# Kernel tuning notes

Measured on AMD Instinct MI355X. Metric: run time of the kernel, lower is better.

## Reference

```python
import jax, jax.numpy as jnp
import numpy as np

DIM = 1024
NUM_HEADS = 16
HEAD_DIM = DIM // NUM_HEADS
SCALE = HEAD_DIM ** -0.5


def setup_inputs() -> dict:
    key = jax.random.key(0)
    ks = jax.random.split(key, 11)
    B, N, M = 8, 1024, 1024
    s = DIM ** -0.5  # init scale for weights
    return {
        "x": jax.random.normal(ks[0], (B, N, DIM), jnp.float32),
        "context": jax.random.normal(ks[1], (B, M, DIM), jnp.float32),
        "Wq": jax.random.normal(ks[2], (DIM, DIM), jnp.float32) * s,
        "bq": jax.random.normal(ks[3], (DIM,), jnp.float32) * 0.01,
        "Wk": jax.random.normal(ks[4], (DIM, DIM), jnp.float32) * s,
        "bk": jax.random.normal(ks[5], (DIM,), jnp.float32) * 0.01,
        "Wv": jax.random.normal(ks[6], (DIM, DIM), jnp.float32) * s,
        "bv": jax.random.normal(ks[7], (DIM,), jnp.float32) * 0.01,
        "Wo": jax.random.normal(ks[8], (DIM, DIM), jnp.float32) * s,
        "bo": jax.random.normal(ks[9], (DIM,), jnp.float32) * 0.01,
    }


def reference(x, context, Wq, bq, Wk, bk, Wv, bv, Wo, bo):
    B, N, _ = x.shape
    M = context.shape[1]
    # Linear projections (torch Linear: x @ W.T + b; here W stored as [in, out])
    q = x @ Wq + bq            # [B, N, DIM]
    k = context @ Wk + bk      # [B, M, DIM]
    v = context @ Wv + bv      # [B, M, DIM]
    # split heads: b n (h d) -> b h n d
    q = q.reshape(B, N, NUM_HEADS, HEAD_DIM).transpose(0, 2, 1, 3)
    k = k.reshape(B, M, NUM_HEADS, HEAD_DIM).transpose(0, 2, 1, 3)
    v = v.reshape(B, M, NUM_HEADS, HEAD_DIM).transpose(0, 2, 1, 3)
    dots = jnp.einsum('bhnd,bhmd->bhnm', q, k) * SCALE
    attn = jax.nn.softmax(dots, axis=-1)
    out = jnp.einsum('bhnm,bhmd->bhnd', attn, v)   # [B, H, N, d]
    out = out.transpose(0, 2, 1, 3).reshape(B, N, DIM)  # b h n d -> b n (h d)
    return out @ Wo + bo
```

## Files before the change

### kernel.cpp

```cpp
#include <hip/hip_runtime.h>

typedef unsigned short u16;
typedef __attribute__((ext_vector_type(8))) short bf16x8;
typedef __attribute__((ext_vector_type(4))) float f32x4;
typedef __attribute__((ext_vector_type(16))) float f32x16;
typedef __attribute__((ext_vector_type(4))) unsigned u32x4;

#define MFMA16 __builtin_amdgcn_mfma_f32_16x16x32_bf16
#define MFMA32 __builtin_amdgcn_mfma_f32_32x32x16_bf16

__device__ __forceinline__ u16 f2b(float f) {
  unsigned u = __builtin_bit_cast(unsigned, f);
  u = (u + 0x7fffu + ((u >> 16) & 1u)) >> 16;
  return (u16)u;
}

__device__ __forceinline__ void gload_lds16(const u16* g, u16* l) {
  __builtin_amdgcn_global_load_lds((const __attribute__((address_space(1))) void*)g,
                                   (__attribute__((address_space(3))) void*)l, 16, 0, 0);
}

__global__ void prep(const float* __restrict__ x, const float* __restrict__ ctx,
                     u16* __restrict__ xb, u16* __restrict__ cb,
                     const float* __restrict__ w0, const float* __restrict__ w1,
                     const float* __restrict__ w2, const float* __restrict__ w3,
                     u16* __restrict__ o0, u16* __restrict__ o1,
                     u16* __restrict__ o2, u16* __restrict__ o3) {
  __shared__ float t[64][65];
  const int z = blockIdx.z;
  const int tid = threadIdx.x;
  if (z < 2) {
    int i = blockIdx.x * blockDim.x + tid;
    const float* in = z ? ctx : x;
    u16* out = z ? cb : xb;
    float4 v = reinterpret_cast<const float4*>(in)[i];
    reinterpret_cast<ushort4*>(out)[i] = make_ushort4(f2b(v.x), f2b(v.y), f2b(v.z), f2b(v.w));
    return;
  }
  const int id = blockIdx.x;
  if (id >= 1024) return;
  const int wsel = id >> 8;
  const float* src = wsel == 0 ? w0 : wsel == 1 ? w1 : wsel == 2 ? w2 : w3;
  u16* dst = wsel == 0 ? o0 : wsel == 1 ? o1 : wsel == 2 ? o2 : o3;
  const int r0 = ((id >> 4) & 15) * 64, c0 = (id & 15) * 64;
  #pragma unroll
  for (int it = 0; it < 4; ++it) {
    int row = it * 16 + (tid >> 4);
    int col = (tid & 15) * 4;
    float4 v = *reinterpret_cast<const float4*>(&src[(size_t)(r0 + row) * 1024 + c0 + col]);
    t[row][col] = v.x; t[row][col + 1] = v.y; t[row][col + 2] = v.z; t[row][col + 3] = v.w;
  }
  __syncthreads();
  #pragma unroll
  for (int it = 0; it < 2; ++it) {
    int c = it * 32 + (tid >> 3);
    int r8 = (tid & 7) * 8;
    u16 tmp[8];
    #pragma unroll
    for (int k = 0; k < 8; ++k) tmp[k] = f2b(t[r8 + k][c]);
    uint4 pk;
    pk.x = (unsigned)tmp[0] | ((unsigned)tmp[1] << 16);
    pk.y = (unsigned)tmp[2] | ((unsigned)tmp[3] << 16);
    pk.z = (unsigned)tmp[4] | ((unsigned)tmp[5] << 16);
    pk.w = (unsigned)tmp[6] | ((unsigned)tmp[7] << 16);
    *reinterpret_cast<uint4*>(&dst[(size_t)(c0 + c) * 1024 + r0 + r8]) = pk;
  }
}

__global__ __launch_bounds__(512, 2) void gemm_qkv256(
    const u16* __restrict__ xb, const u16* __restrict__ cb,
    const u16* __restrict__ Wqt, const u16* __restrict__ Wkt, const u16* __restrict__ Wvt,
    const float* __restrict__ bq, const float* __restrict__ bk, const float* __restrict__ bv,
    u16* __restrict__ Qb, u16* __restrict__ Kf, u16* __restrict__ Vf) {
  __shared__ u16 smem[65536];
  const int tid = threadIdx.x;
  const int lane = tid & 63;
  const int w = tid >> 6;
  const int wr = w >> 2, wc = w & 3;
  const int l16 = lane & 15, g = (lane >> 4) & 3;
  const int z = blockIdx.z;
  const u16* Ain = z == 0 ? xb : cb;
  const u16* Wt = z == 0 ? Wqt : z == 1 ? Wkt : Wvt;
  const float* bias = z == 0 ? bq : z == 1 ? bk : bv;
  const int brow = blockIdx.x * 256, bcol = blockIdx.y * 256;

  int aoff[4], boff[4];
  #pragma unroll
  for (int it = 0; it < 4; ++it) {
    const int c = it * 512 + tid;
    const int l = c & 63;
    const int kk = (c >> 10) * 32 + ((l >> 4) & 3) * 8;
    const int arow = ((c >> 9) & 1) * 128 + ((c >> 6) & 7) * 16 + (l & 15);
    aoff[it] = (brow + arow) * 1024 + kk;
    const int bcolc = ((c >> 8) & 3) * 64 + ((c >> 6) & 3) * 16 + (l & 15);
    boff[it] = (bcol + bcolc) * 1024 + kk;
  }
  auto stageAll = [&](int buf, int t) {
    u16* da = smem + buf * 32768;
    u16* db = da + 16384;
    #pragma unroll
    for (int it = 0; it < 4; ++it)
      gload_lds16(&Ain[(size_t)(aoff[it] + t * 64)], da + (it * 512 + w * 64) * 8);
    #pragma unroll
    for (int it = 0; it < 4; ++it)
      gload_lds16(&Wt[(size_t)(boff[it] + t * 64)], db + (it * 512 + w * 64) * 8);
  };

  f32x4 acc[8][4] = {};
  stageAll(0, 0);
  asm volatile("s_waitcnt vmcnt(0)" ::: "memory");
  __builtin_amdgcn_sched_barrier(0);
  __builtin_amdgcn_s_barrier();

  for (int t = 0; t < 16; ++t) {
    const int buf = t & 1;
    if (t < 15) stageAll(buf ^ 1, t + 1);
    __builtin_amdgcn_sched_barrier(0);
    const u16* As = smem + buf * 32768;
    const u16* Bs = As + 16384;
    #pragma unroll
    for (int ks = 0; ks < 2; ++ks) {
      bf16x8 afr[8], bfr[4];
      #pragma unroll
      for (int nil = 0; nil < 4; ++nil)
        bfr[nil] = *reinterpret_cast<const bf16x8*>(&Bs[(ks * 1024 + wc * 256 + nil * 64 + lane) * 8]);
      #pragma unroll
      for (int mil = 0; mil < 8; ++mil)
        afr[mil] = *reinterpret_cast<const bf16x8*>(&As[(ks * 1024 + wr * 512 + mil * 64 + lane) * 8]);
      __builtin_amdgcn_s_setprio(1);
      #pragma unroll
      for (int mil = 0; mil < 8; ++mil)
        #pragma unroll
        for (int nil = 0; nil < 4; ++nil)
          acc[mil][nil] = MFMA16(afr[mil], bfr[nil], acc[mil][nil], 0, 0, 0);
      __builtin_amdgcn_s_setprio(0);
    }
    __builtin_amdgcn_sched_barrier(0);
    asm volatile("s_waitcnt vmcnt(0)" ::: "memory");
    __builtin_amdgcn_s_barrier();
  }

  u16* T = smem + w * 4608;
  float bz[4];
  #pragma unroll
  for (int ni = 0; ni < 4; ++ni) bz[ni] = bias[bcol + wc * 64 + ni * 16 + l16];
  const float CS = 0.125f * 1.44269504089f;
  const int h = (bcol + wc * 64) >> 6;
  #pragma unroll
  for (int p = 0; p < 2; ++p) {
    if (z < 2) {
      #pragma unroll
      for (int mi4 = 0; mi4 < 4; ++mi4)
        #pragma unroll
        for (int ni = 0; ni < 4; ++ni) {
          f32x4 vv = acc[p * 4 + mi4][ni];
          #pragma unroll
          for (int j = 0; j < 4; ++j) {
            float val = vv[j] + bz[ni];
            if (z == 0) val *= CS;
            T[(mi4 * 16 + g * 4 + j) * 72 + ni * 16 + l16] = f2b(val);
          }
        }
      if (z == 0) {
        #pragma unroll
        for (int it = 0; it < 8; ++it) {
          const int rl = it * 8 + (lane >> 3), c8 = (lane & 7) * 8;
          bf16x8 val = *reinterpret_cast<const bf16x8*>(&T[rl * 72 + c8]);
          *reinterpret_cast<bf16x8*>(
              &Qb[(size_t)(brow + wr * 128 + p * 64 + rl) * 1024 + bcol + wc * 64 + c8]) = val;
        }
      } else {
        #pragma unroll
        for (int it = 0; it < 8; ++it) {
          const int rl = it * 8 + (lane >> 3), c8 = (lane & 7) * 8;
          bf16x8 val = *reinterpret_cast<const bf16x8*>(&T[rl * 72 + c8]);
          const int m = brow + wr * 128 + p * 64 + rl;
          const int bb = m >> 10, kt = (m & 1023) >> 6;
          const int chunk = (c8 >> 4) * 128 + ((m & 63) >> 5) * 64 + ((c8 >> 3) & 1) * 32 + (m & 31);
          *reinterpret_cast<bf16x8*>(&Kf[(((size_t)(bb * 16 + h)) * 16 + kt) * 4096 + chunk * 8]) = val;
        }
      }
    } else {
      #pragma unroll
      for (int mi4 = 0; mi4 < 4; ++mi4)
        #pragma unroll
        for (int ni = 0; ni < 4; ++ni) {
          f32x4 vv = acc[p * 4 + mi4][ni];
          #pragma unroll
          for (int j = 0; j < 4; ++j)
            T[(ni * 16 + l16) * 72 + mi4 * 16 + g * 4 + j] = f2b(vv[j] + bz[ni]);
        }
      #pragma unroll
      for (int it = 0; it < 8; ++it) {
        const int d = it * 8 + (lane >> 3), m8 = (lane & 7) * 8;
        bf16x8 val = *reinterpret_cast<const bf16x8*>(&T[d * 72 + m8]);
        const int m = brow + wr * 128 + p * 64 + m8;
        const int bb = m >> 10, kt = (m & 1023) >> 6;
        const int chunk = (m8 >> 4) * 128 + (d >> 5) * 64 + ((m8 >> 3) & 1) * 32 + (d & 31);
        *reinterpret_cast<bf16x8*>(&Vf[(((size_t)(bb * 16 + h)) * 16 + kt) * 4096 + chunk * 8]) = val;
      }
    }
  }
}

__device__ __forceinline__ void gemm_core(const u16* __restrict__ A, const u16* __restrict__ Wt,
                                          f32x4 (&acc)[4][4], int brow, int bcol,
                                          u16* __restrict__ smem) {
  const int tid = threadIdx.x;
  const int lane = tid & 63;
  const int w = tid >> 6;
  const int wr = w >> 1, wc = w & 1;
  const int l16 = lane & 15, g = lane >> 4;

  auto stage = [&](int buf, int kt) {
    #pragma unroll
    for (int it = 0; it < 4; ++it) {
      int c = it * 256 + tid;
      int row = (c >> 2) & 127;
      int ks = c >> 9;
      int k8 = c & 3;
      const size_t gofs = (size_t)kt * 64 + ks * 32 + k8 * 8;
      gload_lds16(&A[(size_t)(brow + row) * 1024 + gofs],
                  &smem[buf * 8192 + (it * 256 + w * 64) * 8]);
      gload_lds16(&Wt[(size_t)(bcol + row) * 1024 + gofs],
                  &smem[16384 + buf * 8192 + (it * 256 + w * 64) * 8]);
    }
  };

  stage(0, 0);
  __syncthreads();
  int cur = 0;
  for (int kt = 0; kt < 16; ++kt) {
    if (kt < 15) stage(cur ^ 1, kt + 1);
    const u16* As = &smem[cur * 8192];
    const u16* Bs = &smem[16384 + cur * 8192];
    #pragma unroll
    for (int ks = 0; ks < 2; ++ks) {
      bf16x8 a[4], b[4];
      const int kb = ks * 4096 + g * 8;
      #pragma unroll
      for (int mi = 0; mi < 4; ++mi)
        a[mi] = *reinterpret_cast<const bf16x8*>(&As[kb + (wr * 64 + mi * 16 + l16) * 32]);
      #pragma unroll
      for (int ni = 0; ni < 4; ++ni)
        b[ni] = *reinterpret_cast<const bf16x8*>(&Bs[kb + (wc * 64 + ni * 16 + l16) * 32]);
      #pragma unroll
      for (int mi = 0; mi < 4; ++mi)
        #pragma unroll
        for (int ni = 0; ni < 4; ++ni)
          acc[mi][ni] = MFMA16(a[mi], b[ni], acc[mi][ni], 0, 0, 0);
    }
    __syncthreads();
    cur ^= 1;
  }
}

__global__ __launch_bounds__(256, 2) void gemm_o(const u16* __restrict__ A, const u16* __restrict__ Wt,
                                                 const float* __restrict__ bias, float* __restrict__ outp) {
  __shared__ u16 smem[32768];
  const int brow = blockIdx.x * 128, bcol = blockIdx.y * 128;
  f32x4 acc[4][4] = {};
  gemm_core(A, Wt, acc, brow, bcol, smem);
  const int lane = threadIdx.x & 63;
  const int w = threadIdx.x >> 6;
  const int wr = w >> 1, wc = w & 1;
  const int l16 = lane & 15, g = lane >> 4;
  #pragma unroll
  for (int ni = 0; ni < 4; ++ni) {
    const int col = bcol + wc * 64 + ni * 16 + l16;
    const float bz = bias[col];
    #pragma unroll
    for (int mi = 0; mi < 4; ++mi) {
      const int r0 = brow + wr * 64 + mi * 16 + g * 4;
      f32x4 v = acc[mi][ni];
      #pragma unroll
      for (int j = 0; j < 4; ++j) outp[(size_t)(r0 + j) * 1024 + col] = v[j] + bz;
    }
  }
}

__global__ __launch_bounds__(256, 2) void attn2(const u16* __restrict__ Q, const u16* __restrict__ Kf,
                                                const u16* __restrict__ Vf, u16* __restrict__ AO) {
  __shared__ u16 Ks[2][64 * 64];
  __shared__ u16 Vs[2][64 * 64];
  const int tid = threadIdx.x, lane = tid & 63, w = tid >> 6;
  const int l32 = lane & 31, u = lane >> 5;
  const int id = blockIdx.x;
  const int v = (id & 7) * 128 + (id >> 3);
  const int qt = v & 7, h = (v >> 3) & 15, b = v >> 7;
  const int q0 = qt * 128 + w * 32;

  bf16x8 qf[4];
  {
    const u16* qp = &Q[(size_t)(b * 1024 + q0 + l32) * 1024 + h * 64 + u * 8];
    #pragma unroll
    for (int m = 0; m < 4; ++m) qf[m] = *reinterpret_cast<const bf16x8*>(qp + m * 16);
  }

  f32x16 o0 = {}, o1 = {};
  float lr = 0.f;

  const u16* Kbh = Kf + (size_t)(b * 16 + h) * 65536;
  const u16* Vbh = Vf + (size_t)(b * 16 + h) * 65536;

  auto stage = [&](int buf, int kt) {
    #pragma unroll
    for (int it = 0; it < 2; ++it) {
      const int c = (it * 256 + tid) * 8;
      gload_lds16(&Kbh[kt * 4096 + c], &Ks[buf][(it * 256 + w * 64) * 8]);
      gload_lds16(&Vbh[kt * 4096 + c], &Vs[buf][(it * 256 + w * 64) * 8]);
    }
  };

  stage(0, 0);
  __syncthreads();
  int cur = 0;

  for (int kt = 0; kt < 16; ++kt) {
    if (kt < 15) stage(cur ^ 1, kt + 1);

    f32x16 s0 = {}, s1 = {};
    __builtin_amdgcn_s_setprio(1);
    #pragma unroll
    for (int m = 0; m < 4; ++m) {
      bf16x8 k0 = *reinterpret_cast<const bf16x8*>(&Ks[cur][m * 1024 + lane * 8]);
      bf16x8 k1 = *reinterpret_cast<const bf16x8*>(&Ks[cur][m * 1024 + 512 + lane * 8]);
      s0 = MFMA32(k0, qf[m], s0, 0, 0, 0);
      s1 = MFMA32(k1, qf[m], s1, 0, 0, 0);
    }
    __builtin_amdgcn_s_setprio(0);

    unsigned W0[8], W1[8];
    #pragma unroll
    for (int j = 0; j < 8; ++j) {
      const int r = 4 * (j >> 1) + 2 * (j & 1);
      float pa0 = __builtin_amdgcn_exp2f(s0[r]);
      float pb0 = __builtin_amdgcn_exp2f(s0[r + 1]);
      float pa1 = __builtin_amdgcn_exp2f(s1[r]);
      float pb1 = __builtin_amdgcn_exp2f(s1[r + 1]);
      lr += (pa0 + pb0) + (pa1 + pb1);
      asm("v_cvt_pk_bf16_f32 %0, %1, %2" : "=v"(W0[j]) : "v"(pa0), "v"(pb0));
      asm("v_cvt_pk_bf16_f32 %0, %1, %2" : "=v"(W1[j]) : "v"(pa1), "v"(pb1));
    }

    unsigned paw[4][4];
    #pragma unroll
    for (int ks = 0; ks < 4; ++ks) {
      const int ksl = ks & 1;
      #pragma unroll
      for (int p = 0; p < 2; ++p) {
        unsigned x = (ks < 2) ? W0[4 * ksl + p] : W1[4 * ksl + p];
        unsigned y = (ks < 2) ? W0[4 * ksl + 2 + p] : W1[4 * ksl + 2 + p];
        asm("v_permlane32_swap_b32 %0, %1" : "+v"(x), "+v"(y));
        paw[ks][p] = x;
        paw[ks][2 + p] = y;
      }
    }

    __builtin_amdgcn_s_setprio(1);
    #pragma unroll
    for (int ks = 0; ks < 4; ++ks) {
      bf16x8 pa = __builtin_bit_cast(bf16x8, u32x4{paw[ks][0], paw[ks][1], paw[ks][2], paw[ks][3]});
      bf16x8 v0 = *reinterpret_cast<const bf16x8*>(&Vs[cur][ks * 1024 + lane * 8]);
      bf16x8 v1 = *reinterpret_cast<const bf16x8*>(&Vs[cur][ks * 1024 + 512 + lane * 8]);
      o0 = MFMA32(pa, v0, o0, 0, 0, 0);
      o1 = MFMA32(pa, v1, o1, 0, 0, 0);
    }
    __builtin_amdgcn_s_setprio(0);

    __syncthreads();
    cur ^= 1;
  }

  float sum = lr + __shfl_xor(lr, 32);
  float rinv = 1.0f / sum;
  u16* aop = &AO[(size_t)(b * 1024 + q0) * 1024 + h * 64 + l32];
  #pragma unroll
  for (int r = 0; r < 16; ++r) {
    const int ql = (r & 3) + 8 * (r >> 2) + 4 * u;
    int ri_i = __builtin_amdgcn_ds_bpermute((ql + (u << 5)) << 2, __builtin_bit_cast(int, rinv));
    float ri = __builtin_bit_cast(float, ri_i);
    aop[(size_t)ql * 1024] = f2b(o0[r] * ri);
    aop[(size_t)ql * 1024 + 32] = f2b(o1[r] * ri);
  }
}

extern "C" void kernel_launch(void* const* d_in, const int* in_sizes, int n_in,
                              void* d_out, int out_size, void* d_ws, size_t ws_size,
                              hipStream_t stream) {
  const float* x   = (const float*)d_in[0];
  const float* ctx = (const float*)d_in[1];
  const float* Wq  = (const float*)d_in[2];
  const float* bq  = (const float*)d_in[3];
  const float* Wk  = (const float*)d_in[4];
  const float* bk  = (const float*)d_in[5];
  const float* Wv  = (const float*)d_in[6];
  const float* bv  = (const float*)d_in[7];
  const float* Wo  = (const float*)d_in[8];
  const float* bo  = (const float*)d_in[9];
  float* out = (float*)d_out;
  char* ws = (char*)d_ws;

  u16* xb  = (u16*)(ws + (size_t)0);
  u16* cb  = (u16*)(ws + ((size_t)16 << 20));
  u16* Qb  = (u16*)(ws + ((size_t)32 << 20));
  u16* Kf  = (u16*)(ws + ((size_t)48 << 20));
  u16* Vf  = (u16*)(ws + ((size_t)64 << 20));
  u16* Wqt = (u16*)(ws + ((size_t)80 << 20));
  u16* Wkt = (u16*)(ws + ((size_t)82 << 20));
  u16* Wvt = (u16*)(ws + ((size_t)84 << 20));
  u16* Wot = (u16*)(ws + ((size_t)86 << 20));

  prep<<<dim3(8192, 1, 3), 256, 0, stream>>>(x, ctx, xb, cb, Wq, Wk, Wv, Wo, Wqt, Wkt, Wvt, Wot);
  gemm_qkv256<<<dim3(32, 4, 3), 512, 0, stream>>>(xb, cb, Wqt, Wkt, Wvt, bq, bk, bv, Qb, Kf, Vf);
  attn2<<<dim3(1024), 256, 0, stream>>>(Qb, Kf, Vf, xb );
  gemm_o<<<dim3(64, 8), 256, 0, stream>>>(xb, Wot, bo, out);
}
```

Before: 174.9 us.

## Split QKV GEMM staging into half-tiles with finer-grained pipelined loads

```diff
diff --git a/kernel.cpp b/kernel.cpp
--- a/kernel.cpp
+++ b/kernel.cpp
@@ -84,59 +84,114 @@
   const float* bias = z == 0 ? bq : z == 1 ? bk : bv;
   const int brow = blockIdx.x * 256, bcol = blockIdx.y * 256;
 
-  int aoff[4], boff[4];
-  #pragma unroll
-  for (int it = 0; it < 4; ++it) {
+  int aoff[2], boff[2];
+  #pragma unroll
+  for (int it = 0; it < 2; ++it) {
     const int c = it * 512 + tid;
     const int l = c & 63;
-    const int kk = (c >> 10) * 32 + ((l >> 4) & 3) * 8;
-    const int arow = ((c >> 9) & 1) * 128 + ((c >> 6) & 7) * 16 + (l & 15);
-    aoff[it] = (brow + arow) * 1024 + kk;
-    const int bcolc = ((c >> 8) & 3) * 64 + ((c >> 6) & 3) * 16 + (l & 15);
-    boff[it] = (bcol + bcolc) * 1024 + kk;
-  }
-  auto stageAll = [&](int buf, int t) {
-    u16* da = smem + buf * 32768;
-    u16* db = da + 16384;
-    #pragma unroll
-    for (int it = 0; it < 4; ++it)
-      gload_lds16(&Ain[(size_t)(aoff[it] + t * 64)], da + (it * 512 + w * 64) * 8);
-    #pragma unroll
-    for (int it = 0; it < 4; ++it)
-      gload_lds16(&Wt[(size_t)(boff[it] + t * 64)], db + (it * 512 + w * 64) * 8);
+    const int kk = ((c >> 6) & 1) * 32 + ((l >> 4) & 3) * 8;
+    const int rc = ((c >> 7) & 7) * 16 + (l & 15);
+    aoff[it] = (brow + rc) * 1024 + kk;
+    boff[it] = (bcol + rc) * 1024 + kk;
+  }
+  auto stageA = [&](int buf, int ha, int kt) {
+    u16* db = smem + buf * 32768 + ha * 8192;
+    #pragma unroll
+    for (int it = 0; it < 2; ++it)
+      gload_lds16(&Ain[(size_t)(aoff[it] + ha * 131072 + kt * 64)], db + (it * 512 + w * 64) * 8);
   };
+  auto stageB = [&](int buf, int hb, int kt) {
+    u16* db = smem + buf * 32768 + 16384 + hb * 8192;
+    #pragma unroll
+    for (int it = 0; it < 2; ++it)
+      gload_lds16(&Wt[(size_t)(boff[it] + hb * 131072 + kt * 64)], db + (it * 512 + w * 64) * 8);
+  };
 
   f32x4 acc[8][4] = {};
-  stageAll(0, 0);
-  asm volatile("s_waitcnt vmcnt(0)" ::: "memory");
+  stageA(0, 0, 0); stageA(0, 1, 0); stageB(0, 0, 0); stageB(0, 1, 0);
+  stageB(1, 0, 1); stageB(1, 1, 1); stageA(1, 0, 1);
+  asm volatile("s_waitcnt vmcnt(6)" ::: "memory");
   __builtin_amdgcn_sched_barrier(0);
   __builtin_amdgcn_s_barrier();
 
   for (int t = 0; t < 16; ++t) {
-    const int buf = t & 1;
-    if (t < 15) stageAll(buf ^ 1, t + 1);
-    __builtin_amdgcn_sched_barrier(0);
-    const u16* As = smem + buf * 32768;
-    const u16* Bs = As + 16384;
-    #pragma unroll
-    for (int ks = 0; ks < 2; ++ks) {
-      bf16x8 afr[8], bfr[4];
-      #pragma unroll
-      for (int nil = 0; nil < 4; ++nil)
-        bfr[nil] = *reinterpret_cast<const bf16x8*>(&Bs[(ks * 1024 + wc * 256 + nil * 64 + lane) * 8]);
-      #pragma unroll
-      for (int mil = 0; mil < 8; ++mil)
-        afr[mil] = *reinterpret_cast<const bf16x8*>(&As[(ks * 1024 + wr * 512 + mil * 64 + lane) * 8]);
-      __builtin_amdgcn_s_setprio(1);
-      #pragma unroll
-      for (int mil = 0; mil < 8; ++mil)
-        #pragma unroll
-        for (int nil = 0; nil < 4; ++nil)
-          acc[mil][nil] = MFMA16(afr[mil], bfr[nil], acc[mil][nil], 0, 0, 0);
-      __builtin_amdgcn_s_setprio(0);
-    }
-    __builtin_amdgcn_sched_barrier(0);
-    asm volatile("s_waitcnt vmcnt(0)" ::: "memory");
+    const int cur = t & 1;
+    const u16* Ah = smem + cur * 32768 + wr * 8192;
+    const u16* Bh = smem + cur * 32768 + 16384 + (wc >> 1) * 8192;
+    const int bq4 = (wc & 1) * 4;
+    bf16x8 afr[4][2], bfr[4][2];
+
+    #pragma unroll
+    for (int mi = 0; mi < 4; ++mi)
+      #pragma unroll
+      for (int ks = 0; ks < 2; ++ks)
+        afr[mi][ks] = *reinterpret_cast<const bf16x8*>(&Ah[(mi * 128 + ks * 64 + lane) * 8]);
+    #pragma unroll
+    for (int nil = 0; nil < 4; ++nil)
+      #pragma unroll
+      for (int ks = 0; ks < 2; ++ks)
+        bfr[nil][ks] = *reinterpret_cast<const bf16x8*>(&Bh[((bq4 + nil) * 128 + ks * 64 + lane) * 8]);
+    if (t < 15) stageA(cur ^ 1, 1, t + 1);
+    asm volatile("s_waitcnt lgkmcnt(0)" ::: "memory");
+    __builtin_amdgcn_sched_barrier(0);
+    __builtin_amdgcn_s_setprio(1);
+    #pragma unroll
+    for (int mi = 0; mi < 4; ++mi)
+      #pragma unroll
+      for (int nil = 0; nil < 2; ++nil)
+        acc[mi][nil] = MFMA16(afr[mi][1], bfr[nil][1],
+                              MFMA16(afr[mi][0], bfr[nil][0], acc[mi][nil], 0, 0, 0), 0, 0, 0);
+    __builtin_amdgcn_s_setprio(0);
+    __builtin_amdgcn_sched_barrier(0);
+    __builtin_amdgcn_s_barrier();
+
+    if (t < 14) stageB(cur, 0, t + 2);
+    __builtin_amdgcn_s_setprio(1);
+    #pragma unroll
+    for (int mi = 0; mi < 4; ++mi)
+      #pragma unroll
+      for (int nil = 2; nil < 4; ++nil)
+        acc[mi][nil] = MFMA16(afr[mi][1], bfr[nil][1],
+                              MFMA16(afr[mi][0], bfr[nil][0], acc[mi][nil], 0, 0, 0), 0, 0, 0);
+    __builtin_amdgcn_s_setprio(0);
+    __builtin_amdgcn_sched_barrier(0);
+    __builtin_amdgcn_s_barrier();
+
+    #pragma unroll
+    for (int mi = 0; mi < 4; ++mi)
+      #pragma unroll
+      for (int ks = 0; ks < 2; ++ks)
+        afr[mi][ks] = *reinterpret_cast<const bf16x8*>(&Ah[((4 + mi) * 128 + ks * 64 + lane) * 8]);
+    if (t < 14) stageB(cur, 1, t + 2);
+    asm volatile("s_waitcnt lgkmcnt(0)" ::: "memory");
+    __builtin_amdgcn_sched_barrier(0);
+    __builtin_amdgcn_s_setprio(1);
+    #pragma unroll
+    for (int mi = 0; mi < 4; ++mi)
+      #pragma unroll
+      for (int nil = 0; nil < 2; ++nil)
+        acc[4 + mi][nil] = MFMA16(afr[mi][1], bfr[nil][1],
+                                  MFMA16(afr[mi][0], bfr[nil][0], acc[4 + mi][nil], 0, 0, 0), 0, 0, 0);
+    __builtin_amdgcn_s_setprio(0);
+    __builtin_amdgcn_sched_barrier(0);
+    __builtin_amdgcn_s_barrier();
+
+    if (t < 14) stageA(cur, 0, t + 2);
+    if (t < 14) {
+      asm volatile("s_waitcnt vmcnt(6)" ::: "memory");
+    } else if (t == 14) {
+      asm volatile("s_waitcnt vmcnt(0)" ::: "memory");
+    }
+    __builtin_amdgcn_sched_barrier(0);
+    __builtin_amdgcn_s_setprio(1);
+    #pragma unroll
+    for (int mi = 0; mi < 4; ++mi)
+      #pragma unroll
+      for (int nil = 2; nil < 4; ++nil)
+        acc[4 + mi][nil] = MFMA16(afr[mi][1], bfr[nil][1],
+                                  MFMA16(afr[mi][0], bfr[nil][0], acc[4 + mi][nil], 0, 0, 0), 0, 0, 0);
+    __builtin_amdgcn_s_setprio(0);
+    __builtin_amdgcn_sched_barrier(0);
     __builtin_amdgcn_s_barrier();
   }
 
@@ -279,7 +334,7 @@
   }
 }
 
-__global__ __launch_bounds__(256, 2) void attn2(const u16* __restrict__ Q, const u16* __restrict__ Kf,
+__global__ __launch_bounds__(256, 4) void attn2(const u16* __restrict__ Q, const u16* __restrict__ Kf,
                                                 const u16* __restrict__ Vf, u16* __restrict__ AO) {
   __shared__ u16 Ks[2][64 * 64];
   __shared__ u16 Vs[2][64 * 64];
```

Result: faster. 163.6 us (-6.4%).
